# Performance work log

Measured on AMD Instinct MI355X. Metric: run time of the kernel, lower is better.

## Reference

```python
import jax, jax.numpy as jnp
import numpy as np

BATCH = 32
NUM_VARS = 16
SAMPLES = 4096
EMBED_DIM = 128
WINDOW_SIZE = 32
STEP_SIZE = 4
WIDTH = 1.0


def setup_inputs() -> dict:
    key = jax.random.key(0)
    k1, k2, k3, k4, k5 = jax.random.split(key, 5)
    x = jax.random.normal(k1, (BATCH, NUM_VARS, SAMPLES), dtype=jnp.float32)
    # sample-level LSH: num_variables -> embed_dim
    W_sample = jax.random.normal(k2, (NUM_VARS, EMBED_DIM), dtype=jnp.float32)
    b_sample = jax.random.uniform(k3, (EMBED_DIM,), dtype=jnp.float32, minval=0.0, maxval=WIDTH)
    # patch-level LSH: window_size*embed_dim -> embed_dim
    W_patch = jax.random.normal(k4, (WINDOW_SIZE * EMBED_DIM, EMBED_DIM), dtype=jnp.float32)
    b_patch = jax.random.uniform(k5, (EMBED_DIM,), dtype=jnp.float32, minval=0.0, maxval=WIDTH)
    return {"x": x, "W_sample": W_sample, "b_sample": b_sample,
            "W_patch": W_patch, "b_patch": b_patch}


def reference(x, W_sample, b_sample, W_patch, b_patch):
    batch, v, samples = x.shape
    # encode: E2LSH hash of every timestep, fully vectorized over the samples axis
    # enc: [B, S, D]
    enc = jnp.floor((jnp.einsum('bvs,vd->bsd', x, W_sample) + b_sample) / WIDTH)
    # quantize: sliding windows over time, flattened then hashed
    num_tokens = (samples - WINDOW_SIZE) // STEP_SIZE  # matches preallocated tokens
    # idx: [T, W] gather indices for all windows at once
    idx = jnp.arange(num_tokens)[:, None] * STEP_SIZE + jnp.arange(WINDOW_SIZE)[None, :]
    windows = enc[:, idx, :].reshape(batch, num_tokens, WINDOW_SIZE * EMBED_DIM)  # [B, T, W*D]
    tokens = jnp.floor((windows @ W_patch + b_patch) / WIDTH)  # [B, T, D]
    return tokens
```

## Files before the change

### kernel.cpp

```cpp
#include <hip/hip_runtime.h>
#include <hip/hip_bf16.h>
#include <cstdint>

#define BATCH   32
#define NVARS   16
#define SAMPLES 4096
#define EDIM    128
#define NTOK    1016
#define PLELEM  4368

typedef __bf16 bf8_t __attribute__((ext_vector_type(8)));
typedef float  f4_t  __attribute__((ext_vector_type(4)));

__global__ __launch_bounds__(256) void prep_kernel(
    const float* __restrict__ Wp, __hip_bfloat16* __restrict__ WtF)
{
  __shared__ float ls[32][132];
  int tid = threadIdx.x;
  int kb  = blockIdx.x;
  int s = kb >> 3, dlt = kb & 7;
  int kbase = (4 * dlt + (s & 3)) * 128 + (s >> 2) * 32;
#pragma unroll
  for (int r = 0; r < 16; ++r) {
    int idx = tid + r * 256;
    ls[idx >> 7][idx & 127] =
        Wp[(size_t)(kbase + (idx >> 7)) * EDIM + (idx & 127)];
  }
  __syncthreads();
  int g = tid >> 5, l5 = tid & 31;
#pragma unroll
  for (int h = 0; h < 2; ++h) {
    int lane = l5 + h * 32;
    int quad = lane >> 4, l15 = lane & 15;
    int n = g * 16 + l15;
    union { unsigned short u[8]; uint4 v; } pk;
#pragma unroll
    for (int t = 0; t < 8; ++t) {
      __hip_bfloat16 hh = __float2bfloat16(ls[quad * 8 + t][n]);
      pk.u[t] = *(unsigned short*)&hh;
    }
    *(uint4*)(WtF + (size_t)kb * 4096 + g * 512 + lane * 8) = pk.v;
  }
}

__global__ __launch_bounds__(1024, 4) void fused_kernel(
    const float* __restrict__ x,
    const float* __restrict__ Ws,
    const float* __restrict__ bs,
    const __hip_bfloat16* __restrict__ WtF,
    const float* __restrict__ bp,
    float* __restrict__ out)
{
  __shared__ __align__(16) __hip_bfloat16 Apan[16 * PLELEM];
  __shared__ __align__(16) float xTp[2][136][16];

  int tid  = threadIdx.x;
  int lane = tid & 63;
  int wv   = tid >> 6;
  int g2   = wv >> 2;
  int nh   = (wv >> 1) & 1;
  int mh   = wv & 1;
  int b    = blockIdx.x >> 3;
  int t0   = (blockIdx.x & 7) << 7;
  int quad = lane >> 4;
  int l15  = lane & 15;

  const __hip_bfloat16* bg = WtF + (size_t)(nh * 4) * 512 + lane * 8;

  int q4 = tid & 31;
  int eq = q4 >> 3;
  int cq = (q4 >> 1) & 3;
  int hq = q4 & 1;
  int r0 = tid >> 5;

  float w[NVARS][4];
  float bz[4];
  {
    int d0 = q4 * 4;
#pragma unroll
    for (int v = 0; v < NVARS; ++v)
      *(float4*)&w[v][0] = *(const float4*)(Ws + v * EDIM + d0);
    *(float4*)&bz[0] = *(const float4*)(bs + d0);
  }

  int vv = tid & 15, rr = tid >> 4;
  float4 xreg[3];
  {
    const float* xb = x + ((size_t)b * NVARS + vv) * SAMPLES;
    xreg[0] = *(const float4*)(xb + (t0 + rr) * 4);
    xreg[1] = *(const float4*)(xb + (t0 + 64 + rr) * 4);
    if (tid < 128) {
      int s4 = (t0 + 128 + rr) * 4;
      if (s4 > SAMPLES - 4) s4 = SAMPLES - 4;
      xreg[2] = *(const float4*)(xb + s4);
    }
  }

  auto stageX = [&](int p, int buf) {
    float c0 = (p == 0) ? xreg[0].x : (p == 1) ? xreg[0].y
             : (p == 2) ? xreg[0].z : xreg[0].w;
    float c1 = (p == 0) ? xreg[1].x : (p == 1) ? xreg[1].y
             : (p == 2) ? xreg[1].z : xreg[1].w;
    xTp[buf][rr][vv]      = c0;
    xTp[buf][64 + rr][vv] = c1;
    if (tid < 128) {
      float c2 = (p == 0) ? xreg[2].x : (p == 1) ? xreg[2].y
               : (p == 2) ? xreg[2].z : xreg[2].w;
      xTp[buf][128 + rr][vv] = c2;
    }
  };

  auto encTask = [&](int p, int buf, int r) {
    const float* xr = &xTp[buf][r][0];
    float xv[NVARS];
    *(float4*)&xv[0]  = *(const float4*)(xr + 0);
    *(float4*)&xv[4]  = *(const float4*)(xr + 4);
    *(float4*)&xv[8]  = *(const float4*)(xr + 8);
    *(float4*)&xv[12] = *(const float4*)(xr + 12);
    float a0 = bz[0], a1 = bz[1], a2 = bz[2], a3 = bz[3];
#pragma unroll
    for (int v = 0; v < NVARS; ++v) {
      a0 += xv[v] * w[v][0]; a1 += xv[v] * w[v][1];
      a2 += xv[v] * w[v][2]; a3 += xv[v] * w[v][3];
    }
    union { unsigned short us[4]; uint2 q; } pk;
    pk.us[0] = (unsigned short)(__float_as_uint(floorf(a0)) >> 16);
    pk.us[1] = (unsigned short)(__float_as_uint(floorf(a1)) >> 16);
    pk.us[2] = (unsigned short)(__float_as_uint(floorf(a2)) >> 16);
    pk.us[3] = (unsigned short)(__float_as_uint(floorf(a3)) >> 16);
    int phys = (cq + (r >> 1)) & 3;
    char* plbase = (char*)&Apan[(eq * 4 + p) * PLELEM];
    *(uint2*)(plbase + r * 64 + phys * 16 + hq * 8) = pk.q;
  };

  stageX(0, 0);
  __syncthreads();
#pragma unroll
  for (int p = 0; p < 4; ++p) {
    if (p < 3) stageX(p + 1, (p + 1) & 1);
    int buf = p & 1;
#pragma unroll
    for (int j = 0; j < 4; ++j) encTask(p, buf, r0 + 32 * j);
    if (tid < 256) encTask(p, buf, 128 + (tid >> 5));
    __syncthreads();
  }

  f4_t acc[4][4];
  f4_t zero = {0.f, 0.f, 0.f, 0.f};
#pragma unroll
  for (int i = 0; i < 4; ++i)
#pragma unroll
    for (int j = 0; j < 4; ++j) acc[i][j] = zero;

  auto loadB = [&](int kb, uint4* d) {
#pragma unroll
    for (int j = 0; j < 4; ++j)
      d[j] = *(const uint4*)(bg + (size_t)kb * 4096 + j * 512);
  };

  auto loadAF = [&](bf8_t* af, const bf8_t* pA, int dlt) {
    int swz = (quad + ((t0 + mh * 64 + dlt + l15) >> 1)) & 3;
#pragma unroll
    for (int i = 0; i < 4; ++i)
      af[i] = pA[(mh * 64 + dlt + i * 16 + l15) * 4 + swz];
  };

  auto mstep = [&](const bf8_t* af, const uint4* bq_) {
    __builtin_amdgcn_s_setprio(1);
#pragma unroll
    for (int mi = 0; mi < 4; ++mi)
#pragma unroll
      for (int ni = 0; ni < 4; ++ni)
        acc[mi][ni] = __builtin_amdgcn_mfma_f32_16x16x32_bf16(
            af[mi], __builtin_bit_cast(bf8_t, bq_[ni]), acc[mi][ni], 0, 0, 0);
    __builtin_amdgcn_s_setprio(0);
  };

  bf8_t af[4];
  uint4 bq[2][4];
  loadB(g2 * 32 + 0, bq[0]);
  loadB(g2 * 32 + 1, bq[1]);

  for (int ss = 0; ss < 4; ++ss) {
    const bf8_t* pA = (const bf8_t*)&Apan[(g2 * 4 + ss) * PLELEM];
#pragma unroll
    for (int d = 0; d < 8; ++d) {
      int kl = ss * 8 + d;
      loadAF(af, pA, d);
      mstep(af, bq[d & 1]);
      if (kl < 30) loadB(g2 * 32 + kl + 2, bq[d & 1]);
    }
  }

  float* rb2 = (float*)&Apan[0];
  int idx4 = nh * 2 + mh;
  float bias[4];
#pragma unroll
  for (int ni = 0; ni < 4; ++ni) bias[ni] = bp[(nh << 6) + ni * 16 + l15];

#pragma unroll
  for (int rd = 0; rd < 4; ++rd) {
    __syncthreads();
    if (g2 > 0) {
      int slot = ((g2 - 1) * 4 + idx4) * 64 + lane;
#pragma unroll
      for (int ni = 0; ni < 4; ++ni)
        *(f4_t*)&rb2[(size_t)slot * 20 + ni * 4] = acc[rd][ni];
    }
    __syncthreads();
    if (g2 == 0) {
      f4_t s0 = acc[rd][0], s1 = acc[rd][1];
      f4_t s2 = acc[rd][2], s3 = acc[rd][3];
#pragma unroll
      for (int q = 1; q < 4; ++q) {
        int sl = ((q - 1) * 4 + idx4) * 64 + lane;
        s0 += *(const f4_t*)&rb2[(size_t)sl * 20 + 0];
        s1 += *(const f4_t*)&rb2[(size_t)sl * 20 + 4];
        s2 += *(const f4_t*)&rb2[(size_t)sl * 20 + 8];
        s3 += *(const f4_t*)&rb2[(size_t)sl * 20 + 12];
      }
      f4_t sv[4] = {s0, s1, s2, s3};
#pragma unroll
      for (int ni = 0; ni < 4; ++ni)
#pragma unroll
        for (int r = 0; r < 4; ++r) {
          int t = t0 + mh * 64 + rd * 16 + quad * 4 + r;
          if (t < NTOK) {
            int n = (nh << 6) + ni * 16 + l15;
            out[((size_t)b * NTOK + t) * EDIM + n] =
                floorf(sv[ni][r] + bias[ni]);
          }
        }
    }
  }
}

extern "C" void kernel_launch(void* const* d_in, const int* in_sizes, int n_in,
                              void* d_out, int out_size, void* d_ws, size_t ws_size,
                              hipStream_t stream) {
  const float* x  = (const float*)d_in[0];
  const float* Ws = (const float*)d_in[1];
  const float* bs = (const float*)d_in[2];
  const float* Wp = (const float*)d_in[3];
  const float* bp = (const float*)d_in[4];
  float* out = (float*)d_out;

  __hip_bfloat16* WtF = (__hip_bfloat16*)d_ws;

  prep_kernel<<<128, 256, 0, stream>>>(Wp, WtF);
  fused_kernel<<<BATCH * 8, 1024, 0, stream>>>(x, Ws, bs, WtF, bp, out);
}
```

Baseline: 125.2 us.

## Halve token tile per block to 64 and shrink blocks to 512 threads

Each block now handles 64 tokens with 8 waves instead of 128 tokens with 16 waves, which doubles the grid to 512 blocks. The shared A panel shrinks to 72 rows so two blocks can share a CU and overlap one block's encode phase with another's MFMA phase. The double-buffered x staging is replaced by a single buffer with a barrier per phase. In exchange, W_patch fragments are reloaded from L2 by twice as many blocks and there are extra barriers in the encode loop.

```diff
diff --git a/kernel.cpp b/kernel.cpp
--- a/kernel.cpp
+++ b/kernel.cpp
@@ -7,7 +7,8 @@
 #define SAMPLES 4096
 #define EDIM    128
 #define NTOK    1016
-#define PLELEM  4368
+#define NROWS   72
+#define PLELEM  2320
 
 typedef __bf16 bf8_t __attribute__((ext_vector_type(8)));
 typedef float  f4_t  __attribute__((ext_vector_type(4)));
@@ -43,7 +44,7 @@
   }
 }
 
-__global__ __launch_bounds__(1024, 4) void fused_kernel(
+__global__ __launch_bounds__(512, 2) void fused_kernel(
     const float* __restrict__ x,
     const float* __restrict__ Ws,
     const float* __restrict__ bs,
@@ -52,16 +53,15 @@
     float* __restrict__ out)
 {
   __shared__ __align__(16) __hip_bfloat16 Apan[16 * PLELEM];
-  __shared__ __align__(16) float xTp[2][136][16];
+  __shared__ __align__(16) float xT[NROWS][16];
 
   int tid  = threadIdx.x;
   int lane = tid & 63;
   int wv   = tid >> 6;
-  int g2   = wv >> 2;
-  int nh   = (wv >> 1) & 1;
-  int mh   = wv & 1;
-  int b    = blockIdx.x >> 3;
-  int t0   = (blockIdx.x & 7) << 7;
+  int g2   = wv >> 1;
+  int nh   = wv & 1;
+  int b    = blockIdx.x >> 4;
+  int t0   = (blockIdx.x & 15) << 6;
   int quad = lane >> 4;
   int l15  = lane & 15;
 
@@ -88,30 +88,16 @@
   {
     const float* xb = x + ((size_t)b * NVARS + vv) * SAMPLES;
     xreg[0] = *(const float4*)(xb + (t0 + rr) * 4);
-    xreg[1] = *(const float4*)(xb + (t0 + 64 + rr) * 4);
+    xreg[1] = *(const float4*)(xb + (t0 + 32 + rr) * 4);
     if (tid < 128) {
-      int s4 = (t0 + 128 + rr) * 4;
+      int s4 = (t0 + 64 + rr) * 4;
       if (s4 > SAMPLES - 4) s4 = SAMPLES - 4;
       xreg[2] = *(const float4*)(xb + s4);
     }
   }
 
-  auto stageX = [&](int p, int buf) {
-    float c0 = (p == 0) ? xreg[0].x : (p == 1) ? xreg[0].y
-             : (p == 2) ? xreg[0].z : xreg[0].w;
-    float c1 = (p == 0) ? xreg[1].x : (p == 1) ? xreg[1].y
-             : (p == 2) ? xreg[1].z : xreg[1].w;
-    xTp[buf][rr][vv]      = c0;
-    xTp[buf][64 + rr][vv] = c1;
-    if (tid < 128) {
-      float c2 = (p == 0) ? xreg[2].x : (p == 1) ? xreg[2].y
-               : (p == 2) ? xreg[2].z : xreg[2].w;
-      xTp[buf][128 + rr][vv] = c2;
-    }
-  };
-
-  auto encTask = [&](int p, int buf, int r) {
-    const float* xr = &xTp[buf][r][0];
+  auto encTask = [&](int p, int r) {
+    const float* xr = &xT[r][0];
     float xv[NVARS];
     *(float4*)&xv[0]  = *(const float4*)(xr + 0);
     *(float4*)&xv[4]  = *(const float4*)(xr + 4);
@@ -133,15 +119,23 @@
     *(uint2*)(plbase + r * 64 + phys * 16 + hq * 8) = pk.q;
   };
 
-  stageX(0, 0);
-  __syncthreads();
 #pragma unroll
   for (int p = 0; p < 4; ++p) {
-    if (p < 3) stageX(p + 1, (p + 1) & 1);
-    int buf = p & 1;
-#pragma unroll
-    for (int j = 0; j < 4; ++j) encTask(p, buf, r0 + 32 * j);
-    if (tid < 256) encTask(p, buf, 128 + (tid >> 5));
+    float c0 = (p == 0) ? xreg[0].x : (p == 1) ? xreg[0].y
+             : (p == 2) ? xreg[0].z : xreg[0].w;
+    float c1 = (p == 0) ? xreg[1].x : (p == 1) ? xreg[1].y
+             : (p == 2) ? xreg[1].z : xreg[1].w;
+    xT[rr][vv]      = c0;
+    xT[32 + rr][vv] = c1;
+    if (tid < 128) {
+      float c2 = (p == 0) ? xreg[2].x : (p == 1) ? xreg[2].y
+               : (p == 2) ? xreg[2].z : xreg[2].w;
+      xT[64 + rr][vv] = c2;
+    }
+    __syncthreads();
+#pragma unroll
+    for (int j = 0; j < 4; ++j) encTask(p, r0 + 16 * j);
+    if (tid < 256) encTask(p, 64 + (tid >> 5));
     __syncthreads();
   }
 
@@ -159,10 +153,10 @@
   };
 
   auto loadAF = [&](bf8_t* af, const bf8_t* pA, int dlt) {
-    int swz = (quad + ((t0 + mh * 64 + dlt + l15) >> 1)) & 3;
+    int swz = (quad + ((dlt + l15) >> 1)) & 3;
 #pragma unroll
     for (int i = 0; i < 4; ++i)
-      af[i] = pA[(mh * 64 + dlt + i * 16 + l15) * 4 + swz];
+      af[i] = pA[(dlt + i * 16 + l15) * 4 + swz];
   };
 
   auto mstep = [&](const bf8_t* af, const uint4* bq_) {
@@ -193,7 +187,6 @@
   }
 
   float* rb2 = (float*)&Apan[0];
-  int idx4 = nh * 2 + mh;
   float bias[4];
 #pragma unroll
   for (int ni = 0; ni < 4; ++ni) bias[ni] = bp[(nh << 6) + ni * 16 + l15];
@@ -202,7 +195,7 @@
   for (int rd = 0; rd < 4; ++rd) {
     __syncthreads();
     if (g2 > 0) {
-      int slot = ((g2 - 1) * 4 + idx4) * 64 + lane;
+      int slot = ((g2 - 1) * 2 + nh) * 64 + lane;
 #pragma unroll
       for (int ni = 0; ni < 4; ++ni)
         *(f4_t*)&rb2[(size_t)slot * 20 + ni * 4] = acc[rd][ni];
@@ -213,7 +206,7 @@
       f4_t s2 = acc[rd][2], s3 = acc[rd][3];
 #pragma unroll
       for (int q = 1; q < 4; ++q) {
-        int sl = ((q - 1) * 4 + idx4) * 64 + lane;
+        int sl = ((q - 1) * 2 + nh) * 64 + lane;
         s0 += *(const f4_t*)&rb2[(size_t)sl * 20 + 0];
         s1 += *(const f4_t*)&rb2[(size_t)sl * 20 + 4];
         s2 += *(const f4_t*)&rb2[(size_t)sl * 20 + 8];
@@ -224,7 +217,7 @@
       for (int ni = 0; ni < 4; ++ni)
 #pragma unroll
         for (int r = 0; r < 4; ++r) {
-          int t = t0 + mh * 64 + rd * 16 + quad * 4 + r;
+          int t = t0 + rd * 16 + quad * 4 + r;
           if (t < NTOK) {
             int n = (nh << 6) + ni * 16 + l15;
             out[((size_t)b * NTOK + t) * EDIM + n] =
@@ -248,5 +241,5 @@
   __hip_bfloat16* WtF = (__hip_bfloat16*)d_ws;
 
   prep_kernel<<<128, 256, 0, stream>>>(Wp, WtF);
-  fused_kernel<<<BATCH * 8, 1024, 0, stream>>>(x, Ws, bs, WtF, bp, out);
+  fused_kernel<<<BATCH * 16, 512, 0, stream>>>(x, Ws, bs, WtF, bp, out);
 }
```

New measurement: 110.2 us. -12.0%, faster.
